# Kernel tuning notes

Measured on AMD Instinct MI355X. Metric: run time of the kernel, lower is better.

The kernel has to match this reference:

```python
import math
import jax, jax.numpy as jnp
import numpy as np

B, T, E, H = 2, 1024, 1024, 16
D = E // H            # head dim
NREL = 529            # local-relation vocab (max_ary=32)
KMAX = 32             # rel_kmax
RVOC = 64             # tree relation vocab
SQRT = 3.0            # args.sqrt
INF = 10000000000.0
EPS = 1e-06


def _layernorm(x, w, b):
    # TF-style: divide by (std + eps), std is unbiased (torch default ddof=1)
    u = jnp.mean(x, axis=-1, keepdims=True)
    s = jnp.std(x - u, axis=-1, ddof=1, keepdims=True)
    return w * (x - u) / (s + EPS) + b


def _gelu(x):
    return 0.5 * x * (1.0 + jnp.tanh(math.sqrt(2.0 / math.pi) * (x + 0.044715 * x ** 3)))


def setup_inputs() -> dict:
    key = jax.random.key(0)
    ks = jax.random.split(key, 24)
    f32 = jnp.float32
    inp = {
        'x': jax.random.normal(ks[0], (B, T, E), f32),
        'tds': 0.1 * jax.random.normal(ks[1], (B, H, T, T), f32),
        'LR_Q': 0.1 * jax.random.normal(ks[2], (H, NREL, D), f32),
        'LR_K': 0.1 * jax.random.normal(ks[3], (H, NREL, D), f32),
        'rel': jax.random.randint(ks[4], (B, T, T), 0, RVOC, jnp.int32),
        'LR_map': jax.random.randint(ks[5], (B, T, T), 0, NREL, jnp.int32),
        # parameters (Linear weights stored as [in, out])
        'Wqkv': 0.02 * jax.random.normal(ks[6], (E, 3 * E), f32),
        'bqkv': jnp.zeros((3 * E,), f32),
        'Wproj': 0.02 * jax.random.normal(ks[7], (E, E), f32),
        'bproj': jnp.zeros((E,), f32),
        'rel_weights': 1.0 + 0.02 * jax.random.normal(ks[8], (RVOC, H), f32),
        'rel_keys': 0.02 * jax.random.normal(ks[9], (2 * KMAX + 1, D), f32),
        'rel_values': 0.02 * jax.random.normal(ks[10], (2 * KMAX + 1, D), f32),
        'ln1_w': jnp.ones((E,), f32), 'ln1_b': jnp.zeros((E,), f32),
        'ln2_w': jnp.ones((E,), f32), 'ln2_b': jnp.zeros((E,), f32),
        'Wfc': 0.02 * jax.random.normal(ks[11], (E, 4 * E), f32),
        'bfc': jnp.zeros((4 * E,), f32),
        'Wfp': 0.02 * jax.random.normal(ks[12], (4 * E, E), f32),
        'bfp': jnp.zeros((E,), f32),
    }
    return inp


def reference(x, tds, LR_Q, LR_K, Wqkv, bqkv, Wproj, bproj, rel_weights,
              rel_keys, rel_values, ln1_w, ln1_b, ln2_w, ln2_b,
              Wfc, bfc, Wfp, bfp, rel, LR_map):
    inv_sqrt_d = 1.0 / math.sqrt(D)
    # --- attention branch ---
    h = _layernorm(x, ln1_w, ln1_b)
    qkv = h @ Wqkv + bqkv                                   # [B,T,3E]
    q, k, v = jnp.split(qkv, 3, axis=-1)
    q = q.reshape(B, T, H, D).transpose(0, 2, 1, 3)         # [B,H,T,D]
    k = k.reshape(B, T, H, D).transpose(0, 2, 1, 3)
    v = v.reshape(B, T, H, D).transpose(0, 2, 1, 3)

    w = jnp.einsum('bhid,bhjd->bhij', q, k)                 # raw scores
    # sequential relative keys (rel_ids buffer)
    idx = jnp.arange(T)
    rel_ids = jnp.clip(idx[None, :] - idx[:, None], -KMAX, KMAX) + KMAX  # [T,T]
    relk = rel_keys[rel_ids]                                # [T,T,D]
    w = w + jnp.einsum('bhid,ijd->bhij', q, relk)
    w = w * inv_sqrt_d                                      # self.scale

    bmask = jnp.tril(jnp.ones((T, T), jnp.float32))         # causal bias buffer
    # tree relation (multiplicative, additive=False)
    rele = rel_weights[rel].transpose(0, 3, 1, 2)           # [B,H,T,T]
    w = w * (rele * bmask)
    # TD tree positional encoding
    w = w + tds
    # local relation terms with gather
    lmap = jnp.broadcast_to(LR_map[:, None], (B, H, T, T))
    lr1 = jnp.einsum('bhid,hnd->bhin', q, LR_K) * inv_sqrt_d  # [B,H,T,N]
    lr1 = jnp.take_along_axis(lr1, lmap, axis=-1)             # [B,H,T,T]
    lr2 = jnp.einsum('hnd,bhjd->bhnj', LR_Q, k) * inv_sqrt_d  # [B,H,N,T]
    lr2 = jnp.take_along_axis(lr2, lmap, axis=-2)             # [B,H,T,T]
    w = (w + lr1 + lr2) / math.sqrt(SQRT)

    w = w * bmask - INF * (1.0 - bmask)
    p = jax.nn.softmax(w, axis=-1)
    ret = jnp.einsum('bhij,bhjd->bhid', p, v)
    relv = rel_values[rel_ids]                               # [T,T,D]
    ret = ret + jnp.einsum('bhij,ijd->bhid', p, relv)
    a = ret.transpose(0, 2, 1, 3).reshape(B, T, E) @ Wproj + bproj
    x = x + a
    # --- MLP branch ---
    h2 = _layernorm(x, ln2_w, ln2_b)
    m = _gelu(h2 @ Wfc + bfc) @ Wfp + bfp
    return x + m
```

## Files before the change

kernel.cpp:

```cpp
#include <hip/hip_runtime.h>
#include <hip/hip_bf16.h>
#include <math.h>

typedef __hip_bfloat16 bf16;
typedef __attribute__((ext_vector_type(8))) short short8;
typedef __attribute__((ext_vector_type(4))) float f32x4;

#define B_    2
#define T_    1024
#define E_    1024
#define H_    16
#define NREL_ 529
#define E3_   3072
#define E4_   4096

#define AS1 __attribute__((address_space(1)))
#define AS3 __attribute__((address_space(3)))

__device__ __forceinline__ void gload16(const void* g, void* l) {
  __builtin_amdgcn_global_load_lds((const AS1 unsigned int*)g,
                                   (AS3 unsigned int*)l, 16, 0, 0);
}
__device__ __forceinline__ float b2f(short s) {
  union { unsigned u; float f; } c; c.u = ((unsigned)(unsigned short)s) << 16; return c.f;
}
__device__ __forceinline__ float ldmix(const void* p, size_t i, int isbf) {
  return isbf ? b2f(((const short*)p)[i]) : ((const float*)p)[i];
}
__device__ __forceinline__ void stmix(void* p, size_t i, int isbf, float v) {
  if (isbf) ((bf16*)p)[i] = __float2bfloat16(v);
  else      ((float*)p)[i] = v;
}
__device__ __forceinline__ float waveReduceSum(float v) {
#pragma unroll
  for (int o = 32; o > 0; o >>= 1) v += __shfl_xor(v, o);
  return v;
}

__global__ void probe_kernel(const unsigned* __restrict__ w, int* __restrict__ flag) {
  if (threadIdx.x == 0 && blockIdx.x == 0) *flag = (w[0] == 0x3F803F80u) ? 1 : 0;
}

__global__ __launch_bounds__(256) void ln_kernel(const void* __restrict__ x,
    const void* __restrict__ w, const void* __restrict__ bia, bf16* __restrict__ out,
    const int* __restrict__ flag, int xIsBf) {
  __shared__ float scr[4];
  int isbf = *flag;
  int xbf = isbf | xIsBf;
  int row = blockIdx.x, t = threadIdx.x;
  size_t base = (size_t)row * E_;
  float v[4]; float sum = 0.f;
#pragma unroll
  for (int u = 0; u < 4; u++) { v[u] = ldmix(x, base + u * 256 + t, xbf); sum += v[u]; }
  sum = waveReduceSum(sum);
  if ((t & 63) == 0) scr[t >> 6] = sum;
  __syncthreads();
  sum = scr[0] + scr[1] + scr[2] + scr[3];
  float mean = sum * (1.f / E_);
  float ss = 0.f;
#pragma unroll
  for (int u = 0; u < 4; u++) { float d = v[u] - mean; ss += d * d; }
  ss = waveReduceSum(ss);
  __syncthreads();
  if ((t & 63) == 0) scr[t >> 6] = ss;
  __syncthreads();
  ss = scr[0] + scr[1] + scr[2] + scr[3];
  float istd = 1.f / (sqrtf(ss * (1.f / (E_ - 1))) + 1e-6f);
#pragma unroll
  for (int u = 0; u < 4; u++) {
    int c = u * 256 + t;
    out[base + c] = __float2bfloat16(ldmix(w, c, isbf) * (v[u] - mean) * istd
                                     + ldmix(bia, c, isbf));
  }
}

__global__ __launch_bounds__(256) void tconv_kernel(const void* __restrict__ W,
    bf16* __restrict__ Wt, int K, int N, const int* __restrict__ flag) {
  __shared__ float tile[32][33];
  int isbf = *flag;
  int k0 = blockIdx.x * 32, n0 = blockIdx.y * 32;
  int t = threadIdx.x, c = t & 31, r0 = t >> 5;
#pragma unroll
  for (int rr = 0; rr < 4; rr++) {
    int r = r0 + rr * 8;
    tile[r][c] = ldmix(W, (size_t)(k0 + r) * N + n0 + c, isbf);
  }
  __syncthreads();
#pragma unroll
  for (int rr = 0; rr < 4; rr++) {
    int r = r0 + rr * 8;
    Wt[(size_t)(n0 + r) * K + k0 + c] = __float2bfloat16(tile[c][r]);
  }
}

__global__ __launch_bounds__(256) void vt_kernel(const bf16* __restrict__ qkv,
    bf16* __restrict__ vT) {
  __shared__ short tile[32][33];
  int j0 = blockIdx.x * 32, d0 = blockIdx.y * 32;
  int bh = blockIdx.z; int b = bh >> 4, h = bh & 15;
  int t = threadIdx.x, c = t & 31, r0 = t >> 5;
#pragma unroll
  for (int rr = 0; rr < 4; rr++) {
    int r = r0 + rr * 8;
    tile[r][c] = ((const short*)qkv)[(size_t)(b * T_ + j0 + r) * E3_ + 2 * E_ + h * 64 + d0 + c];
  }
  __syncthreads();
#pragma unroll
  for (int rr = 0; rr < 4; rr++) {
    int r = r0 + rr * 8;
    ((short*)vT)[((size_t)(b * H_ + h) * 64 + d0 + r) * T_ + j0 + c] = tile[c][r];
  }
}

__global__ __launch_bounds__(256) void prep_kernel(const void* __restrict__ relk,
    const void* __restrict__ relv, bf16* __restrict__ relkB, bf16* __restrict__ relvT,
    const int* __restrict__ flag) {
  int isbf = *flag, t = threadIdx.x;
  for (int i = t; i < 48 * 64; i += 256) {
    int tt = i >> 6, d = i & 63;
    relkB[i] = __float2bfloat16(tt < 33 ? ldmix(relk, (size_t)tt * 64 + d, isbf) : 0.f);
  }
  for (int i = t; i < 64 * 64; i += 256) {
    int d = i >> 6, tt = i & 63;
    relvT[i] = __float2bfloat16(tt < 33 ? ldmix(relv, (size_t)tt * 64 + d, isbf) : 0.f);
  }
}

__global__ __launch_bounds__(256) void padlr_kernel(const void* __restrict__ LR,
    bf16* __restrict__ LRp, const int* __restrict__ flag) {
  int isbf = *flag;
  int h = blockIdx.y, t = threadIdx.x;
  int n = blockIdx.x * 4 + (t >> 6), d = t & 63;
  float v = (n < NREL_) ? ldmix(LR, ((size_t)h * NREL_ + n) * 64 + d, isbf) : 0.f;
  LRp[((size_t)h * 640 + n) * 64 + d] = __float2bfloat16(v);
}

__device__ void mgemm_body(const bf16* __restrict__ A, int lda,
    const bf16* __restrict__ Wt, const void* __restrict__ bias,
    const void* __restrict__ resid, void* __restrict__ C, int ldc,
    int K, int nmax, int act, int outbf, int resbf, float cscale,
    int bm, int bn, int isbf) {
  __shared__ __align__(16) short As[128 * 64];
  __shared__ __align__(16) short Bs[128 * 64];
  int t = threadIdx.x, w = t >> 6, lane = t & 63;
  int wm = (w & 1) * 64, wn = (w >> 1) * 64;
  int cg = ((lane & 7) ^ ((lane >> 3) & 7)) * 8;
  int rsub = lane >> 3;
  const bf16* gA = A  + (size_t)(bm + w * 32 + rsub) * lda + cg;
  const bf16* gB = Wt + (size_t)(bn + w * 32 + rsub) * K + cg;
  short* lA = As + (w * 32) * 64;
  short* lB = Bs + (w * 32) * 64;
  f32x4 acc[4][4] = {};
  int lm = lane & 15, kq = lane >> 4;
  for (int k0 = 0; k0 < K; k0 += 64) {
#pragma unroll
    for (int i = 0; i < 4; i++) {
      gload16(gA + (size_t)i * 8 * lda + k0, lA + i * 8 * 64);
      gload16(gB + (size_t)i * 8 * K + k0, lB + i * 8 * 64);
    }
    __syncthreads();
#pragma unroll
    for (int ks = 0; ks < 2; ks++) {
      short8 af[4], bf_[4];
#pragma unroll
      for (int mi = 0; mi < 4; mi++) {
        int row = wm + mi * 16 + lm;
        int ci = (ks * 4 + kq) ^ (lm & 7);
        af[mi] = *(const short8*)&As[row * 64 + ci * 8];
      }
#pragma unroll
      for (int ni = 0; ni < 4; ni++) {
        int row = wn + ni * 16 + lm;
        int ci = (ks * 4 + kq) ^ (lm & 7);
        bf_[ni] = *(const short8*)&Bs[row * 64 + ci * 8];
      }
#pragma unroll
      for (int mi = 0; mi < 4; mi++)
#pragma unroll
        for (int ni = 0; ni < 4; ni++)
          acc[mi][ni] = __builtin_amdgcn_mfma_f32_16x16x32_bf16(
              af[mi], bf_[ni], acc[mi][ni], 0, 0, 0);
    }
    __syncthreads();
  }
  int rq = lane >> 4;
#pragma unroll
  for (int ni = 0; ni < 4; ni++) {
    int col = bn + wn + ni * 16 + lm;
    if (col < nmax) {
      float bv = bias ? ldmix(bias, col, isbf) : 0.f;
#pragma unroll
      for (int mi = 0; mi < 4; mi++) {
#pragma unroll
        for (int r = 0; r < 4; r++) {
          int rowg = bm + wm + mi * 16 + rq * 4 + r;
          float v = acc[mi][ni][r] * cscale + bv;
          if (act == 1) {
            float uu = 0.7978845608028654f * (v + 0.044715f * v * v * v);
            v = 0.5f * v * (1.f + tanhf(uu));
          }
          size_t off = (size_t)rowg * ldc + col;
          if (resid) v += ldmix(resid, off, resbf);
          stmix(C, off, outbf, v);
        }
      }
    }
  }
}

__global__ __launch_bounds__(256) void mgemm_kernel(const bf16* __restrict__ A,
    const bf16* __restrict__ Wt, const void* __restrict__ bias,
    const void* __restrict__ resid, void* __restrict__ C,
    int N, int K, int act, int mode, const int* __restrict__ flag) {
  int isbf = *flag;
  int outbf = (mode == 1) ? isbf : 1;
  int resbf = (mode == 1) ? 1 : isbf;
  mgemm_body(A, K, Wt, bias, resid, C, N, K, N, act, outbf, resbf, 1.f,
             blockIdx.y * 128, blockIdx.x * 128, isbf);
}

__global__ __launch_bounds__(256) void lrmm_kernel(const bf16* __restrict__ qkv,
    const bf16* __restrict__ LRp, bf16* __restrict__ out, int koff, int b0) {
  int z = blockIdx.z, h = z & 15, b = b0 + (z >> 4);
  const bf16* A = qkv + (size_t)(b * T_) * E3_ + h * 64 + koff;
  const bf16* Wt = LRp + (size_t)h * 640 * 64;
  bf16* C = out + (size_t)z * T_ * NREL_;
  mgemm_body(A, E3_, Wt, nullptr, nullptr, C, NREL_, 64, NREL_, 0, 1, 1, 0.125f,
             blockIdx.y * 128, blockIdx.x * 128, 0);
}

#define MF(a, b, c) __builtin_amdgcn_mfma_f32_16x16x32_bf16(a, b, c, 0, 0, 0)
__global__ __launch_bounds__(64, 2) void attn_kernel(const bf16* __restrict__ qkv,
    const void* __restrict__ tds, const void* __restrict__ relw,
    const int* __restrict__ rel, const int* __restrict__ lmap,
    const bf16* __restrict__ lr1, const bf16* __restrict__ lr2,
    const bf16* __restrict__ vT, const bf16* __restrict__ relkB,
    const bf16* __restrict__ relvT, bf16* __restrict__ retE,
    int b0, const int* __restrict__ flag) {
  __shared__ __align__(16) short sQ[16 * 64];
  __shared__ __align__(16) short sK[32 * 64];
  __shared__ __align__(16) short sVt[64 * 32];
  __shared__ __align__(16) short sP[16 * 40];
  __shared__ __align__(16) short sPb[16 * 72];
  __shared__ float qrkT[16 * 36];
  __shared__ float mT[16], lT[16];

  int isbf = *flag;
  int lane = threadIdx.x;
  int h = blockIdx.x;
  int y = blockIdx.y;
  int it = (y & 1) ? (63 - (y >> 1)) : (y >> 1);
  int b = b0 + blockIdx.z;
  int i0 = it * 16;
  int col = lane & 15, q = lane >> 4;

  {
    int r = lane >> 3, c = lane & 7;
#pragma unroll
    for (int i = 0; i < 2; i++) {
      int row = i * 8 + r;
      gload16((const short*)qkv + (size_t)(b * T_ + i0 + row) * E3_ + h * 64
              + ((c ^ (row & 7)) * 8), sQ + i * 8 * 64);
    }
  }
  __builtin_amdgcn_s_waitcnt(0x0F70);
  short8 qf[2];
#pragma unroll
  for (int ko = 0; ko < 2; ko++)
    qf[ko] = *(const short8*)&sQ[col * 64 + (((ko * 4 + q) ^ (col & 7)) * 8)];

#pragma unroll
  for (int nt = 0; nt < 3; nt++) {
    f32x4 z = {};
    const short* rp = (const short*)relkB + (size_t)(nt * 16 + col) * 64 + q * 8;
    z = MF(qf[0], *(const short8*)rp, z);
    z = MF(qf[1], *(const short8*)(rp + 32), z);
    int t = nt * 16 + col;
    if (t < 33) {
#pragma unroll
      for (int r = 0; r < 4; r++) qrkT[(q * 4 + r) * 36 + t] = z[r];
    }
  }

  f32x4 acc[4] = {};
  float m_r[4], l_r[4];
#pragma unroll
  for (int r = 0; r < 4; r++) { m_r[r] = -3e38f; l_r[r] = 0.f; }

  int ntile = ((i0 + 15) >> 5) + 1;
  const short* kbase = (const short*)qkv + (size_t)b * T_ * E3_ + E_ + h * 64;
  const short* vtb   = (const short*)vT + ((size_t)(b * H_ + h) * 64) * T_;
  const int* rel0  = rel  + (size_t)b * T_ * T_;
  const int* map0  = lmap + (size_t)b * T_ * T_;
  size_t tdsbase = ((size_t)(b * H_ + h) * T_) * T_;
  const short* lr1h = (const short*)lr1 + (size_t)(blockIdx.z * H_ + h) * T_ * NREL_;
  const short* lr2h = (const short*)lr2 + (size_t)(blockIdx.z * H_ + h) * T_ * NREL_;

  int r8 = lane >> 3, c8 = lane & 7;
  int r4 = lane >> 2, c4 = lane & 3;
  short8 kreg[4], vreg[4];
  int nrel[8], nmap[8]; float ntds[8];
  int crel[8], cmap[8]; float ctds[8];

#pragma unroll
  for (int i = 0; i < 4; i++) {
    int row = i * 8 + r8;
    kreg[i] = *(const short8*)(kbase + (size_t)row * E3_ + ((c8 ^ (row & 7)) * 8));
  }
#pragma unroll
  for (int i = 0; i < 4; i++) {
    int row = i * 16 + r4;
    vreg[i] = *(const short8*)(vtb + (size_t)row * T_ + ((c4 ^ (row & 3)) * 8));
  }
#pragma unroll
  for (int nt = 0; nt < 2; nt++)
#pragma unroll
    for (int r = 0; r < 4; r++) {
      int e = nt * 4 + r;
      int j = nt * 16 + col;
      int i = i0 + q * 4 + r;
      size_t o = (size_t)i * T_ + j;
      nrel[e] = rel0[o]; nmap[e] = map0[o]; ntds[e] = ldmix(tds, tdsbase + o, isbf);
    }
#pragma unroll
  for (int i = 0; i < 4; i++) {
    int row = i * 8 + r8;
    *(short8*)&sK[row * 64 + c8 * 8] = kreg[i];
  }
#pragma unroll
  for (int i = 0; i < 4; i++) {
    int row = i * 16 + r4;
    *(short8*)&sVt[row * 32 + c4 * 8] = vreg[i];
  }
#pragma unroll
  for (int e = 0; e < 8; e++) { crel[e] = nrel[e]; cmap[e] = nmap[e]; ctds[e] = ntds[e]; }

  for (int jt = 0; jt < ntile; jt++) {
    int j0 = jt * 32;
    int more = (jt + 1 < ntile);
    if (more) {
      int j0n = j0 + 32;
#pragma unroll
      for (int i = 0; i < 4; i++) {
        int row = i * 8 + r8;
        kreg[i] = *(const short8*)(kbase + (size_t)(j0n + row) * E3_
                                   + ((c8 ^ (row & 7)) * 8));
      }
#pragma unroll
      for (int i = 0; i < 4; i++) {
        int row = i * 16 + r4;
        vreg[i] = *(const short8*)(vtb + (size_t)row * T_ + j0n
                                   + ((c4 ^ (row & 3)) * 8));
      }
#pragma unroll
      for (int nt = 0; nt < 2; nt++)
#pragma unroll
        for (int r = 0; r < 4; r++) {
          int e = nt * 4 + r;
          int j = j0n + nt * 16 + col;
          int i = i0 + q * 4 + r;
          size_t o = (size_t)i * T_ + j;
          nrel[e] = rel0[o]; nmap[e] = map0[o]; ntds[e] = ldmix(tds, tdsbase + o, isbf);
        }
    }

    f32x4 sA[2];
#pragma unroll
    for (int nt = 0; nt < 2; nt++) {
      f32x4 z = {};
#pragma unroll
      for (int ko = 0; ko < 2; ko++) {
        short8 kf = *(const short8*)&sK[(nt * 16 + col) * 64
                                        + (((ko * 4 + q) ^ (col & 7)) * 8)];
        z = MF(qf[ko], kf, z);
      }
      sA[nt] = z;
    }
    float sv[2][4];
#pragma unroll
    for (int nt = 0; nt < 2; nt++) {
      int j = j0 + nt * 16 + col;
#pragma unroll
      for (int r = 0; r < 4; r++) {
        int i = i0 + q * 4 + r;
        int e = nt * 4 + r;
        float x = -1e10f;
        if (j <= i) {
          int rid = j - i + 32; rid = rid < 0 ? 0 : rid;
          float s1 = (sA[nt][r] + qrkT[(q * 4 + r) * 36 + rid]) * 0.125f;
          s1 *= ldmix(relw, (size_t)crel[e] * H_ + h, isbf);
          s1 += ctds[e];
          int mm = cmap[e];
          s1 = (s1 + b2f(lr1h[(size_t)i * NREL_ + mm])
                   + b2f(lr2h[(size_t)j * NREL_ + mm])) * 0.57735026918962576f;
          x = s1;
        }
        sv[nt][r] = x;
      }
    }
#pragma unroll
    for (int r = 0; r < 4; r++) {
      float tm = fmaxf(sv[0][r], sv[1][r]);
#pragma unroll
      for (int o = 1; o < 16; o <<= 1) tm = fmaxf(tm, __shfl_xor(tm, o));
      float mn = fmaxf(m_r[r], tm);
      float al = __expf(m_r[r] - mn);
      m_r[r] = mn;
#pragma unroll
      for (int dt = 0; dt < 4; dt++) acc[dt][r] *= al;
      float p0 = __expf(sv[0][r] - mn), p1 = __expf(sv[1][r] - mn);
      float rs = p0 + p1;
#pragma unroll
      for (int o = 1; o < 16; o <<= 1) rs += __shfl_xor(rs, o);
      l_r[r] = l_r[r] * al + rs;
      ((bf16*)sP)[(q * 4 + r) * 40 + col]      = __float2bfloat16(p0);
      ((bf16*)sP)[(q * 4 + r) * 40 + 16 + col] = __float2bfloat16(p1);
    }
    short8 pf = *(const short8*)&sP[col * 40 + q * 8];
#pragma unroll
    for (int dt = 0; dt < 4; dt++) {
      int row = dt * 16 + col;
      short8 vf = *(const short8*)&sVt[row * 32 + ((q ^ (row & 3)) * 8)];
      acc[dt] = MF(pf, vf, acc[dt]);
    }

    if (more) {
#pragma unroll
      for (int i = 0; i < 4; i++) {
        int row = i * 8 + r8;
        *(short8*)&sK[row * 64 + c8 * 8] = kreg[i];
      }
#pragma unroll
      for (int i = 0; i < 4; i++) {
        int row = i * 16 + r4;
        *(short8*)&sVt[row * 32 + c4 * 8] = vreg[i];
      }
#pragma unroll
      for (int e = 0; e < 8; e++) { crel[e] = nrel[e]; cmap[e] = nmap[e]; ctds[e] = ntds[e]; }
    }
  }

#pragma unroll
  for (int r = 0; r < 4; r++) {
    float inv = 1.f / l_r[r];
#pragma unroll
    for (int dt = 0; dt < 4; dt++) acc[dt][r] *= inv;
  }
  if (col == 0) {
#pragma unroll
    for (int r = 0; r < 4; r++) { mT[q * 4 + r] = m_r[r]; lT[q * 4 + r] = l_r[r]; }
  }
  for (int k2 = lane; k2 < 16 * 36; k2 += 64) ((unsigned*)sPb)[k2] = 0u;
  int brow = col, ig = i0 + brow;
  short8 qv[8];
#pragma unroll
  for (int c2 = 0; c2 < 8; c2++)
    qv[c2] = *(const short8*)&sQ[brow * 64 + ((c2 ^ (brow & 7)) * 8)];
  float mfin = mT[brow], lfin = lT[brow];
  float sump = 0.f;
#pragma unroll
  for (int e = 0; e < 8; e++) {
    int tt = q * 8 + e + 1;
    int j = ig + tt - 32;
    if (j >= 0) {
      const short* kj = kbase + (size_t)j * E3_;
      float dacc = 0.f;
#pragma unroll
      for (int c2 = 0; c2 < 8; c2++) {
        short8 kk = *(const short8*)(kj + c2 * 8);
        short8 qq = qv[c2];
#pragma unroll
        for (int e2 = 0; e2 < 8; e2++) dacc += b2f(qq[e2]) * b2f(kk[e2]);
      }
      float s1 = (dacc + qrkT[brow * 36 + tt]) * 0.125f;
      s1 *= ldmix(relw, (size_t)rel0[(size_t)ig * T_ + j] * H_ + h, isbf);
      s1 += ldmix(tds, tdsbase + (size_t)ig * T_ + j, isbf);
      int mm = map0[(size_t)ig * T_ + j];
      s1 = (s1 + b2f(lr1h[(size_t)ig * NREL_ + mm])
               + b2f(lr2h[(size_t)j * NREL_ + mm])) * 0.57735026918962576f;
      float pn = __expf(s1 - mfin) / lfin;
      ((bf16*)sPb)[brow * 72 + tt] = __float2bfloat16(pn);
      sump += pn;
    }
  }
  sump += __shfl_xor(sump, 16); sump += __shfl_xor(sump, 32);
  if (q == 0) ((bf16*)sPb)[brow * 72] = __float2bfloat16(fmaxf(1.f - sump, 0.f));
  short8 pbf[2];
#pragma unroll
  for (int ko = 0; ko < 2; ko++)
    pbf[ko] = *(const short8*)&sPb[col * 72 + ko * 32 + q * 8];
#pragma unroll
  for (int dt = 0; dt < 4; dt++) {
#pragma unroll
    for (int ko = 0; ko < 2; ko++) {
      int row = dt * 16 + col;
      short8 rv = *(const short8*)((const short*)relvT + (size_t)row * 64
                                   + (ko * 4 + q) * 8);
      acc[dt] = MF(pbf[ko], rv, acc[dt]);
    }
  }
#pragma unroll
  for (int dt = 0; dt < 4; dt++)
#pragma unroll
    for (int r = 0; r < 4; r++)
      retE[(size_t)(b * T_ + i0 + q * 4 + r) * E_ + h * 64 + dt * 16 + col]
          = __float2bfloat16(acc[dt][r]);
}

extern "C" void kernel_launch(void* const* d_in, const int* in_sizes, int n_in,
                              void* d_out, int out_size, void* d_ws, size_t ws_size,
                              hipStream_t stream) {
  (void)in_sizes; (void)n_in; (void)out_size;
  const void* x    = d_in[0];
  const void* tds  = d_in[1];
  const void* LRQ  = d_in[2];
  const void* LRK  = d_in[3];
  const int*  rel  = (const int*)d_in[4];
  const int*  lmap = (const int*)d_in[5];
  const void* Wqkv = d_in[6];
  const void* bqkv = d_in[7];
  const void* Wproj= d_in[8];
  const void* bproj= d_in[9];
  const void* relw = d_in[10];
  const void* relk = d_in[11];
  const void* relv = d_in[12];
  const void* ln1w = d_in[13];
  const void* ln1b = d_in[14];
  const void* ln2w = d_in[15];
  const void* ln2b = d_in[16];
  const void* Wfc  = d_in[17];
  const void* bfc  = d_in[18];
  const void* Wfp  = d_in[19];
  const void* bfp  = d_in[20];

  char* wsp = (char*)d_ws;
  bf16* qkv   = (bf16*)(wsp + 0);
  bf16* WfcT  = (bf16*)(wsp + 0);
  bf16* h     = (bf16*)(wsp + 12582912);
  bf16* LRKp  = (bf16*)(wsp + 12582912);
  bf16* LRQp  = (bf16*)(wsp + 13893632);
  bf16* x2    = (bf16*)(wsp + 12582912);
  bf16* WqkvT = (bf16*)(wsp + 16777216);
  bf16* lr1p  = (bf16*)(wsp + 16777216);
  bf16* WfpT  = (bf16*)(wsp + 16777216);
  bf16* lr2p  = (bf16*)(wsp + 34111488);
  bf16* WprojT= (bf16*)(wsp + 34111488);
  bf16* g     = (bf16*)(wsp + 34111488);
  bf16* retE  = (bf16*)(wsp + 51445760);
  bf16* h2    = (bf16*)(wsp + 51445760);
  int*  flag  = (int*) (wsp + 55640064);
  bf16* vT    = (bf16*)(wsp + 55640320);
  bf16* relkB = (bf16*)(wsp + 59834624);
  bf16* relvT = (bf16*)(wsp + 59840768);
  bf16* lr2d  = (bf16*)(wsp + 59848960);
  bool dual = ws_size >= 94517504u;

  probe_kernel<<<1, 64, 0, stream>>>((const unsigned*)ln1w, flag);
  prep_kernel<<<1, 256, 0, stream>>>(relk, relv, relkB, relvT, flag);

  tconv_kernel<<<dim3(E_ / 32, E3_ / 32), 256, 0, stream>>>(Wqkv, WqkvT, E_, E3_, flag);
  ln_kernel<<<B_ * T_, 256, 0, stream>>>(x, ln1w, ln1b, h, flag, 0);
  mgemm_kernel<<<dim3(E3_ / 128, (B_ * T_) / 128), 256, 0, stream>>>(
      h, WqkvT, bqkv, nullptr, qkv, E3_, E_, 0, 0, flag);
  vt_kernel<<<dim3(T_ / 32, 2, B_ * H_), 256, 0, stream>>>(qkv, vT);
  padlr_kernel<<<dim3(160, H_), 256, 0, stream>>>(LRK, LRKp, flag);
  padlr_kernel<<<dim3(160, H_), 256, 0, stream>>>(LRQ, LRQp, flag);

  if (dual) {
    lrmm_kernel<<<dim3(5, 8, 32), 256, 0, stream>>>(qkv, LRKp, lr1p, 0, 0);
    lrmm_kernel<<<dim3(5, 8, 32), 256, 0, stream>>>(qkv, LRQp, lr2d, E_, 0);
    attn_kernel<<<dim3(H_, 64, B_), 64, 0, stream>>>(qkv, tds, relw, rel, lmap,
        lr1p, lr2d, vT, relkB, relvT, retE, 0, flag);
  } else {
    for (int b = 0; b < B_; b++) {
      lrmm_kernel<<<dim3(5, 8, 16), 256, 0, stream>>>(qkv, LRKp, lr1p, 0, b);
      lrmm_kernel<<<dim3(5, 8, 16), 256, 0, stream>>>(qkv, LRQp, lr2p, E_, b);
      attn_kernel<<<dim3(H_, 64, 1), 64, 0, stream>>>(qkv, tds, relw, rel, lmap,
          lr1p, lr2p, vT, relkB, relvT, retE, b, flag);
    }
  }

  tconv_kernel<<<dim3(E_ / 32, E_ / 32), 256, 0, stream>>>(Wproj, WprojT, E_, E_, flag);
  tconv_kernel<<<dim3(E_ / 32, E4_ / 32), 256, 0, stream>>>(Wfc, WfcT, E_, E4_, flag);
  tconv_kernel<<<dim3(E4_ / 32, E_ / 32), 256, 0, stream>>>(Wfp, WfpT, E4_, E_, flag);

  mgemm_kernel<<<dim3(E_ / 128, (B_ * T_) / 128), 256, 0, stream>>>(
      retE, WprojT, bproj, x, x2, E_, E_, 0, 0, flag);
  ln_kernel<<<B_ * T_, 256, 0, stream>>>(x2, ln2w, ln2b, h2, flag, 1);
  mgemm_kernel<<<dim3(E4_ / 128, (B_ * T_) / 128), 256, 0, stream>>>(
      h2, WfcT, bfc, nullptr, g, E4_, E_, 1, 0, flag);
  mgemm_kernel<<<dim3(E_ / 128, (B_ * T_) / 128), 256, 0, stream>>>(
      g, WfpT, bfp, x2, d_out, E_, E4_, 0, 1, flag);
}
```

Before: 891.2 us.

## Pipeline gathers two tiles ahead and skip masked index loads

Restructures the attention kernel's prefetch into a two-stage software pipeline. Index loads (rel, LR_map, tds) now run two key tiles ahead, and the dependent gathers (rel weight, lr1, lr2) run one tile ahead, so the gather latency no longer sits inside the score computation. Loads for masked (j>i) positions are skipped. This adds register pressure in a 64-thread, 2-block launch, which could cause spills or lower occupancy.

Measured after the change: 891.1 us. Within noise of the previous version (-0.0%).

```diff
diff --git a/kernel.cpp b/kernel.cpp
--- a/kernel.cpp
+++ b/kernel.cpp
@@ -230,6 +230,35 @@
 }
 
 #define MF(a, b, c) __builtin_amdgcn_mfma_f32_16x16x32_bf16(a, b, c, 0, 0, 0)
+
+#define LOADIDX(J0X, RA, MA, TDA) do { \
+  _Pragma("unroll") for (int nt2 = 0; nt2 < 2; nt2++) { \
+    _Pragma("unroll") for (int r2 = 0; r2 < 4; r2++) { \
+      int e2 = nt2 * 4 + r2; \
+      int jj = (J0X) + nt2 * 16 + col; \
+      int ii = i0 + q * 4 + r2; \
+      RA[e2] = 0; MA[e2] = 0; TDA[e2] = 0.f; \
+      if (jj <= ii) { \
+        size_t oo = (size_t)ii * T_ + jj; \
+        RA[e2] = rel0[oo]; MA[e2] = map0[oo]; \
+        TDA[e2] = ldmix(tds, tdsbase + oo, isbf); \
+      } } } \
+} while (0)
+
+#define GATHVAL(J0X, RA, MA, WA, V1A, V2A) do { \
+  _Pragma("unroll") for (int nt2 = 0; nt2 < 2; nt2++) { \
+    _Pragma("unroll") for (int r2 = 0; r2 < 4; r2++) { \
+      int e2 = nt2 * 4 + r2; \
+      int jj = (J0X) + nt2 * 16 + col; \
+      int ii = i0 + q * 4 + r2; \
+      WA[e2] = 1.f; V1A[e2] = 0.f; V2A[e2] = 0.f; \
+      if (jj <= ii) { \
+        WA[e2] = ldmix(relw, (size_t)RA[e2] * H_ + h, isbf); \
+        V1A[e2] = b2f(lr1h[(size_t)ii * NREL_ + MA[e2]]); \
+        V2A[e2] = b2f(lr2h[(size_t)jj * NREL_ + MA[e2]]); \
+      } } } \
+} while (0)
+
 __global__ __launch_bounds__(64, 2) void attn_kernel(const bf16* __restrict__ qkv,
     const void* __restrict__ tds, const void* __restrict__ relw,
     const int* __restrict__ rel, const int* __restrict__ lmap,
@@ -300,8 +329,11 @@
   int r4 = lane >> 2, c4 = lane & 3;
   short8 kreg[4], vreg[4];
   int nrel[8], nmap[8]; float ntds[8];
-  int crel[8], cmap[8]; float ctds[8];
-
+  int trel[8], tmap[8]; float ttds[8];
+  float cw[8], c1[8], c2[8], ctds[8];
+  float nw[8], n1[8], n2[8];
+
+  LOADIDX(0, nrel, nmap, ntds);
 #pragma unroll
   for (int i = 0; i < 4; i++) {
     int row = i * 8 + r8;
@@ -312,16 +344,10 @@
     int row = i * 16 + r4;
     vreg[i] = *(const short8*)(vtb + (size_t)row * T_ + ((c4 ^ (row & 3)) * 8));
   }
-#pragma unroll
-  for (int nt = 0; nt < 2; nt++)
-#pragma unroll
-    for (int r = 0; r < 4; r++) {
-      int e = nt * 4 + r;
-      int j = nt * 16 + col;
-      int i = i0 + q * 4 + r;
-      size_t o = (size_t)i * T_ + j;
-      nrel[e] = rel0[o]; nmap[e] = map0[o]; ntds[e] = ldmix(tds, tdsbase + o, isbf);
-    }
+  GATHVAL(0, nrel, nmap, cw, c1, c2);
+#pragma unroll
+  for (int e = 0; e < 8; e++) ctds[e] = ntds[e];
+  if (ntile > 1) LOADIDX(32, nrel, nmap, ntds);
 #pragma unroll
   for (int i = 0; i < 4; i++) {
     int row = i * 8 + r8;
@@ -332,8 +358,6 @@
     int row = i * 16 + r4;
     *(short8*)&sVt[row * 32 + c4 * 8] = vreg[i];
   }
-#pragma unroll
-  for (int e = 0; e < 8; e++) { crel[e] = nrel[e]; cmap[e] = nmap[e]; ctds[e] = ntds[e]; }
 
   for (int jt = 0; jt < ntile; jt++) {
     int j0 = jt * 32;
@@ -352,16 +376,8 @@
         vreg[i] = *(const short8*)(vtb + (size_t)row * T_ + j0n
                                    + ((c4 ^ (row & 3)) * 8));
       }
-#pragma unroll
-      for (int nt = 0; nt < 2; nt++)
-#pragma unroll
-        for (int r = 0; r < 4; r++) {
-          int e = nt * 4 + r;
-          int j = j0n + nt * 16 + col;
-          int i = i0 + q * 4 + r;
-          size_t o = (size_t)i * T_ + j;
-          nrel[e] = rel0[o]; nmap[e] = map0[o]; ntds[e] = ldmix(tds, tdsbase + o, isbf);
-        }
+      GATHVAL(j0n, nrel, nmap, nw, n1, n2);
+      if (jt + 2 < ntile) LOADIDX(j0 + 64, trel, tmap, ttds);
     }
 
     f32x4 sA[2];
@@ -388,11 +404,8 @@
         if (j <= i) {
           int rid = j - i + 32; rid = rid < 0 ? 0 : rid;
           float s1 = (sA[nt][r] + qrkT[(q * 4 + r) * 36 + rid]) * 0.125f;
-          s1 *= ldmix(relw, (size_t)crel[e] * H_ + h, isbf);
-          s1 += ctds[e];
-          int mm = cmap[e];
-          s1 = (s1 + b2f(lr1h[(size_t)i * NREL_ + mm])
-                   + b2f(lr2h[(size_t)j * NREL_ + mm])) * 0.57735026918962576f;
+          s1 = s1 * cw[e] + ctds[e];
+          s1 = (s1 + c1[e] + c2[e]) * 0.57735026918962576f;
           x = s1;
         }
         sv[nt][r] = x;
@@ -436,7 +449,15 @@
         *(short8*)&sVt[row * 32 + c4 * 8] = vreg[i];
       }
 #pragma unroll
-      for (int e = 0; e < 8; e++) { crel[e] = nrel[e]; cmap[e] = nmap[e]; ctds[e] = ntds[e]; }
+      for (int e = 0; e < 8; e++) {
+        cw[e] = nw[e]; c1[e] = n1[e]; c2[e] = n2[e]; ctds[e] = ntds[e];
+      }
+      if (jt + 2 < ntile) {
+#pragma unroll
+        for (int e = 0; e < 8; e++) {
+          nrel[e] = trel[e]; nmap[e] = tmap[e]; ntds[e] = ttds[e];
+        }
+      }
     }
   }
 
```
